# Kernel tuning notes

Measured on AMD Instinct MI355X. Metric: run time of the kernel, lower is better.

The kernel has to match this reference:

```python
import jax, jax.numpy as jnp
import numpy as np

# Block structure (mirrors init_kwargs)
K = 8            # number of blocks
BLK = 1024       # per-block in/out width
TOTAL = K * BLK  # total_dim = 8192
INPUT_IDX = [(i * BLK, (i + 1) * BLK) for i in range(K)]
OUTPUT_IDX = [(((i + 1) % K) * BLK, ((i + 1) % K + 1) * BLK) for i in range(K)]
BATCH = 4096


def setup_inputs() -> dict:
    key = jax.random.key(0)
    k1, k2, k3, k4 = jax.random.split(key, 4)
    x = jax.random.normal(k1, (BATCH, TOTAL), dtype=jnp.float32)
    v = jax.random.normal(k2, (BATCH, TOTAL), dtype=jnp.float32)
    # Per-block Linear params; nn.Linear default init ~ U(-1/sqrt(in), 1/sqrt(in))
    bound = 1.0 / np.sqrt(BLK)
    W = jax.random.uniform(k3, (K, BLK, BLK), dtype=jnp.float32, minval=-bound, maxval=bound)  # [K, out, in]
    b = jax.random.uniform(k4, (K, BLK), dtype=jnp.float32, minval=-bound, maxval=bound)
    return {"x": x, "v": v, "W": W, "b": b}


def reference(x, v, W, b):
    # hidden = act(v)
    hidden = jnp.tanh(v)
    # All input blocks are a uniform partition -> batch the K small GEMMs as one grouped contraction.
    h = hidden.reshape(BATCH, K, BLK)                      # [B, K, in]
    y = jnp.einsum("bki,koi->bko", h, W) + b               # [B, K, out]
    # Scatter-accumulate each block output into its padded position, plus residual x.
    result = x
    for i, (o0, o1) in enumerate(OUTPUT_IDX):
        result = result.at[:, o0:o1].add(y[:, i])
    return result
```

## Files before the change

kernel.cpp:

```cpp
#include <hip/hip_runtime.h>
#include <hip/hip_bf16.h>
#include <stdint.h>

#define BATCH 4096
#define KGRP  8
#define BLK   1024
#define TOTAL 8192

typedef __attribute__((ext_vector_type(8))) short short8;
typedef __attribute__((ext_vector_type(4))) float f32x4;

#define AS1 __attribute__((address_space(1)))
#define AS3 __attribute__((address_space(3)))


__device__ __forceinline__ unsigned short f2bf(float f) {
    union { float f; uint32_t u; } c; c.f = f;
    uint32_t u = c.u;
    u += 0x7fffu + ((u >> 16) & 1u);
    return (unsigned short)(u >> 16);
}

__device__ __forceinline__ float fast_tanh(float x) {
    float e = __expf(2.0f * x);
    return 1.0f - 2.0f / (e + 1.0f);
}


__global__ void k_prep(const float4* __restrict__ v, ushort4* __restrict__ H,
                       const float4* __restrict__ W, ushort4* __restrict__ Wb) {
    const int b = blockIdx.x;
    if (b < 2048) {
        const int n4 = BATCH * TOTAL / 4;
        for (int i = b * 256 + threadIdx.x; i < n4; i += 2048 * 256) {
            float4 f = v[i];
            ushort4 o;
            o.x = f2bf(fast_tanh(f.x)); o.y = f2bf(fast_tanh(f.y));
            o.z = f2bf(fast_tanh(f.z)); o.w = f2bf(fast_tanh(f.w));
            H[i] = o;
        }
    } else {
        const int n4 = KGRP * BLK * BLK / 4;
        for (int i = (b - 2048) * 256 + threadIdx.x; i < n4; i += 512 * 256) {
            float4 f = W[i];
            ushort4 o;
            o.x = f2bf(f.x); o.y = f2bf(f.y); o.z = f2bf(f.z); o.w = f2bf(f.w);
            Wb[i] = o;
        }
    }
}


__device__ __forceinline__ void stage_a(const unsigned short* Asrc0, char* ldsp,
                                        uint32_t bufb, uint32_t sb, int kt, int half) {
#pragma unroll
    for (int h = 0; h < 2; ++h) {
        const int c = half + h * 2;
        __builtin_amdgcn_global_load_lds(
            (const AS1 uint32_t*)(Asrc0 + (size_t)(c * 64) * TOTAL + kt * 64),
            (AS3 uint32_t*)(ldsp + bufb + c * 8192 + sb), 16, 0, 0);
    }
}

__device__ __forceinline__ void stage_b(const unsigned short* Bsrc0, char* ldsp,
                                        uint32_t bufb, uint32_t sb, int kt) {
#pragma unroll
    for (int c = 0; c < 4; ++c) {
        __builtin_amdgcn_global_load_lds(
            (const AS1 uint32_t*)(Bsrc0 + (size_t)(c * 64) * BLK + kt * 64),
            (AS3 uint32_t*)(ldsp + bufb + 32768u + c * 8192 + sb), 16, 0, 0);
    }
}

template<int N> __device__ __forceinline__ void waitvm() {
    if constexpr (N == 0)       asm volatile("s_waitcnt vmcnt(0)" ::: "memory");
    else if constexpr (N == 2)  asm volatile("s_waitcnt vmcnt(2)" ::: "memory");
    else if constexpr (N == 8)  asm volatile("s_waitcnt vmcnt(8)" ::: "memory");
    else if constexpr (N == 12) asm volatile("s_waitcnt vmcnt(12)" ::: "memory");
}

template<int M0>
__device__ __forceinline__ void mfma_phase(const short8 am[2][2], const short8 bfr[4][2],
                                           f32x4 (*acc)[4]) {
    __builtin_amdgcn_s_barrier();
    __builtin_amdgcn_s_setprio(1);
#pragma unroll
    for (int i = 0; i < 2; ++i)
#pragma unroll
        for (int n = 0; n < 4; ++n)
#pragma unroll
            for (int ks = 0; ks < 2; ++ks)
                acc[M0 + i][n] = __builtin_amdgcn_mfma_f32_16x16x32_bf16(am[i][ks], bfr[n][ks], acc[M0 + i][n], 0, 0, 0);
    __builtin_amdgcn_s_setprio(0);
}

template<bool SA13, bool SB, bool SA02, int W1, int W3>
__device__ __forceinline__ void tile_body(int kt, uint32_t bufb, char* ldsp,
                                          uint32_t aRow, uint32_t bRow, const uint32_t* kc,
                                          f32x4 (*acc)[4],
                                          const unsigned short* Asrc0, const unsigned short* Bsrc0,
                                          uint32_t sb) {
    const char* Lb = ldsp + bufb;
    short8 bfr[4][2], am[2][2];

#pragma unroll
    for (int n = 0; n < 4; ++n)
#pragma unroll
        for (int ks = 0; ks < 2; ++ks)
            bfr[n][ks] = *(const short8*)(Lb + bRow + n * 2048 + kc[ks]);
#pragma unroll
    for (int i = 0; i < 2; ++i)
#pragma unroll
        for (int ks = 0; ks < 2; ++ks)
            am[i][ks] = *(const short8*)(Lb + aRow + i * 2048 + kc[ks]);
    if constexpr (SA13) stage_a(Asrc0, ldsp, bufb ^ 65536u, sb, kt + 1, 1);
    mfma_phase<0>(am, bfr, acc);
    __builtin_amdgcn_s_barrier();

#pragma unroll
    for (int i = 0; i < 2; ++i)
#pragma unroll
        for (int ks = 0; ks < 2; ++ks)
            am[i][ks] = *(const short8*)(Lb + aRow + (2 + i) * 2048 + kc[ks]);
    if constexpr (SB) stage_b(Bsrc0, ldsp, bufb, sb, kt + 2);
    mfma_phase<2>(am, bfr, acc);
    waitvm<W1>();
    __builtin_amdgcn_s_barrier();

#pragma unroll
    for (int i = 0; i < 2; ++i)
#pragma unroll
        for (int ks = 0; ks < 2; ++ks)
            am[i][ks] = *(const short8*)(Lb + aRow + (4 + i) * 2048 + kc[ks]);
    if constexpr (SA02) stage_a(Asrc0, ldsp, bufb, sb, kt + 2, 0);
    mfma_phase<4>(am, bfr, acc);
    __builtin_amdgcn_s_barrier();

#pragma unroll
    for (int i = 0; i < 2; ++i)
#pragma unroll
        for (int ks = 0; ks < 2; ++ks)
            am[i][ks] = *(const short8*)(Lb + aRow + (6 + i) * 2048 + kc[ks]);
    mfma_phase<6>(am, bfr, acc);
    if constexpr (W3 >= 0) {
        waitvm<W3>();
        __builtin_amdgcn_s_barrier();
        __builtin_amdgcn_sched_barrier(0);
    }
}

__global__ __launch_bounds__(512, 2)
void k_gemm(const unsigned short* __restrict__ H, const unsigned short* __restrict__ Wb,
            const float* __restrict__ x, const float* __restrict__ bias,
            float* __restrict__ out) {
    __shared__ __attribute__((aligned(1024))) char lds[131072];
    char* ldsp = lds;

    const int bid   = blockIdx.x;
    const int g     = bid & 7;
    const int slot  = bid >> 3;
    const int mtile = slot >> 2;
    const int ntile = slot & 3;

    const int tid  = threadIdx.x;
    const int lane = tid & 63;
    const int w    = tid >> 6;
    const int wr   = w >> 2;
    const int wc   = w & 3;

    uint32_t kc[2];
#pragma unroll
    for (int ks = 0; ks < 2; ++ks)
        kc[ks] = (uint32_t)((ks * 64 + ((lane >> 4) << 4)) ^ ((lane & 7) << 4));
    const uint32_t aRow = (uint32_t)(wr * 128 + (lane & 15)) * 128u;
    const uint32_t bRow = 32768u + (uint32_t)(wc * 64 + (lane & 15)) * 128u;

    const int sRow = tid >> 3;
    const int sCol = (((lane & 7) ^ ((lane >> 3) & 7)) << 3);
    const unsigned short* Asrc0 = H  + ((size_t)(mtile * 256) + sRow) * TOTAL + (size_t)g * BLK + sCol;
    const unsigned short* Bsrc0 = Wb + ((size_t)g * BLK * BLK) + ((size_t)(ntile * 256) + sRow) * BLK + sCol;
    const uint32_t sb = (uint32_t)(w << 10);

    f32x4 acc[8][4];
#pragma unroll
    for (int m = 0; m < 8; ++m)
#pragma unroll
        for (int n = 0; n < 4; ++n) acc[m][n] = (f32x4){0.f, 0.f, 0.f, 0.f};

    stage_b(Bsrc0, ldsp, 0u, sb, 0);
    stage_a(Asrc0, ldsp, 0u, sb, 0, 0);
    stage_a(Asrc0, ldsp, 0u, sb, 0, 1);
    stage_b(Bsrc0, ldsp, 65536u, sb, 1);
    stage_a(Asrc0, ldsp, 65536u, sb, 1, 0);
    waitvm<8>();
    __builtin_amdgcn_s_barrier();
    __builtin_amdgcn_sched_barrier(0);

    uint32_t cur = 0;
#pragma unroll 1
    for (int kt = 0; kt < 14; ++kt) {
        tile_body<true, true, true, 12, 8>(kt, cur << 16, ldsp, aRow, bRow, kc, acc, Asrc0, Bsrc0, sb);
        cur ^= 1u;
    }
    tile_body<true, false, false, 8, 2>(14, cur << 16, ldsp, aRow, bRow, kc, acc, Asrc0, Bsrc0, sb);
    cur ^= 1u;
    tile_body<false, false, false, 0, -1>(15, cur << 16, ldsp, aRow, bRow, kc, acc, Asrc0, Bsrc0, sb);

    const int gout = (g + 1) & 7;
    const int row0 = mtile * 256 + wr * 128 + ((lane >> 4) << 2);
    const int colL = ntile * 256 + wc * 64 + (lane & 15);
    float bv[4];
#pragma unroll
    for (int n = 0; n < 4; ++n) bv[n] = bias[g * BLK + colL + n * 16];
#pragma unroll
    for (int m = 0; m < 8; ++m) {
#pragma unroll
        for (int j = 0; j < 4; ++j) {
            const int row = row0 + m * 16 + j;
            const size_t base = (size_t)row * TOTAL + (size_t)gout * BLK;
#pragma unroll
            for (int n = 0; n < 4; ++n) {
                const size_t idx = base + colL + n * 16;
                out[idx] = x[idx] + bv[n] + acc[m][n][j];
            }
        }
    }
}


__global__ void k_naive(const float* __restrict__ x, const float* __restrict__ v,
                        const float* __restrict__ W, const float* __restrict__ b,
                        float* __restrict__ out) {
    __shared__ float hv[BLK];
    const int bid = blockIdx.x;
    const int quarter = bid & 3;
    const int g = (bid >> 2) & 7;
    const int row = bid >> 5;
    for (int i = threadIdx.x; i < BLK; i += 256)
        hv[i] = tanhf(v[(size_t)row * TOTAL + g * BLK + i]);
    __syncthreads();
    const int o = quarter * 256 + threadIdx.x;
    const float* wrow = W + ((size_t)g * BLK + o) * BLK;
    float s = 0.f;
    for (int i = 0; i < BLK; ++i) s += hv[i] * wrow[i];
    const size_t oi = (size_t)row * TOTAL + (size_t)((g + 1) & 7) * BLK + o;
    out[oi] = x[oi] + b[g * BLK + o] + s;
}


extern "C" void kernel_launch(void* const* d_in, const int* in_sizes, int n_in,
                              void* d_out, int out_size, void* d_ws, size_t ws_size,
                              hipStream_t stream) {
    const float* x = (const float*)d_in[0];
    const float* v = (const float*)d_in[1];
    const float* W = (const float*)d_in[2];
    const float* b = (const float*)d_in[3];
    float* out = (float*)d_out;

    const size_t needH = (size_t)BATCH * TOTAL * sizeof(unsigned short);
    const size_t needW = (size_t)KGRP * BLK * BLK * sizeof(unsigned short);

    if (ws_size >= needH + needW) {
        unsigned short* H  = (unsigned short*)d_ws;
        unsigned short* Wb = (unsigned short*)((char*)d_ws + needH);
        k_prep<<<2560, 256, 0, stream>>>((const float4*)v, (ushort4*)H,
                                         (const float4*)W, (ushort4*)Wb);
        k_gemm<<<512, 512, 0, stream>>>(H, Wb, x, b, out);
    } else {
        k_naive<<<BATCH * KGRP * 4, 256, 0, stream>>>(x, v, W, b, out);
    }
}
```

Baseline: 153.8 us.

## Use 1024-thread blocks with K=32 tiles and LDS-staged coalesced epilogue

The GEMM kernel moves from 512 to 1024 threads per block with a smaller per-wave accumulator tile (4x4 instead of 8x4) and K-step 32 instead of 64, changing the double-buffered LDS staging and swizzle accordingly. The epilogue now transposes accumulators through LDS so each lane writes float4 rows, making the x read and out write coalesced and vectorized. This aims for more waves to hide latency and cheaper output stores, at the cost of twice as many K iterations and barriers, and less data reuse per wave.

```diff
diff --git a/kernel.cpp b/kernel.cpp
--- a/kernel.cpp
+++ b/kernel.cpp
@@ -51,109 +51,64 @@
 }
 
 
-__device__ __forceinline__ void stage_a(const unsigned short* Asrc0, char* ldsp,
-                                        uint32_t bufb, uint32_t sb, int kt, int half) {
-#pragma unroll
-    for (int h = 0; h < 2; ++h) {
-        const int c = half + h * 2;
-        __builtin_amdgcn_global_load_lds(
-            (const AS1 uint32_t*)(Asrc0 + (size_t)(c * 64) * TOTAL + kt * 64),
-            (AS3 uint32_t*)(ldsp + bufb + c * 8192 + sb), 16, 0, 0);
-    }
-}
-
-__device__ __forceinline__ void stage_b(const unsigned short* Bsrc0, char* ldsp,
-                                        uint32_t bufb, uint32_t sb, int kt) {
-#pragma unroll
-    for (int c = 0; c < 4; ++c) {
-        __builtin_amdgcn_global_load_lds(
-            (const AS1 uint32_t*)(Bsrc0 + (size_t)(c * 64) * BLK + kt * 64),
-            (AS3 uint32_t*)(ldsp + bufb + 32768u + c * 8192 + sb), 16, 0, 0);
-    }
+__device__ __forceinline__ void gload16(const unsigned short* src, char* dst) {
+    __builtin_amdgcn_global_load_lds((const AS1 uint32_t*)src, (AS3 uint32_t*)dst, 16, 0, 0);
 }
 
 template<int N> __device__ __forceinline__ void waitvm() {
-    if constexpr (N == 0)       asm volatile("s_waitcnt vmcnt(0)" ::: "memory");
-    else if constexpr (N == 2)  asm volatile("s_waitcnt vmcnt(2)" ::: "memory");
-    else if constexpr (N == 8)  asm volatile("s_waitcnt vmcnt(8)" ::: "memory");
-    else if constexpr (N == 12) asm volatile("s_waitcnt vmcnt(12)" ::: "memory");
-}
-
-template<int M0>
-__device__ __forceinline__ void mfma_phase(const short8 am[2][2], const short8 bfr[4][2],
-                                           f32x4 (*acc)[4]) {
+    if constexpr (N == 0)      asm volatile("s_waitcnt vmcnt(0)" ::: "memory");
+    else if constexpr (N == 1) asm volatile("s_waitcnt vmcnt(1)" ::: "memory");
+    else if constexpr (N == 2) asm volatile("s_waitcnt vmcnt(2)" ::: "memory");
+}
+
+template<bool SA, bool SB, int W>
+__device__ __forceinline__ void tile_body(int kt, char* ldsp,
+                                          uint32_t aRowB, uint32_t bRowB, uint32_t kc,
+                                          f32x4 (*acc)[4],
+                                          const unsigned short* Asrc, const unsigned short* Bsrc,
+                                          uint32_t sdst) {
+    const uint32_t bufb = (uint32_t)(kt & 1) * 32768u;
+    const uint32_t nbuf = bufb ^ 32768u;
+    const char* Lb = ldsp + bufb;
+
+    short8 bfr[4], am[2];
+
+#pragma unroll
+    for (int n = 0; n < 4; ++n)
+        bfr[n] = *(const short8*)(Lb + bRowB + n * 1024 + kc);
+#pragma unroll
+    for (int i = 0; i < 2; ++i)
+        am[i] = *(const short8*)(Lb + aRowB + i * 1024 + kc);
+    if constexpr (SA) gload16(Asrc + (kt + 1) * 32, ldsp + nbuf + sdst);
+#pragma unroll
+    for (int i = 0; i < 2; ++i)
+#pragma unroll
+        for (int n = 0; n < 4; ++n)
+            acc[i][n] = __builtin_amdgcn_mfma_f32_16x16x32_bf16(am[i], bfr[n], acc[i][n], 0, 0, 0);
     __builtin_amdgcn_s_barrier();
-    __builtin_amdgcn_s_setprio(1);
+    __builtin_amdgcn_sched_barrier(0);
+
+#pragma unroll
+    for (int i = 0; i < 2; ++i)
+        am[i] = *(const short8*)(Lb + aRowB + (2 + i) * 1024 + kc);
+    if constexpr (SB) gload16(Bsrc + (kt + 2) * 32, ldsp + bufb + 16384u + sdst);
 #pragma unroll
     for (int i = 0; i < 2; ++i)
 #pragma unroll
         for (int n = 0; n < 4; ++n)
-#pragma unroll
-            for (int ks = 0; ks < 2; ++ks)
-                acc[M0 + i][n] = __builtin_amdgcn_mfma_f32_16x16x32_bf16(am[i][ks], bfr[n][ks], acc[M0 + i][n], 0, 0, 0);
-    __builtin_amdgcn_s_setprio(0);
-}
-
-template<bool SA13, bool SB, bool SA02, int W1, int W3>
-__device__ __forceinline__ void tile_body(int kt, uint32_t bufb, char* ldsp,
-                                          uint32_t aRow, uint32_t bRow, const uint32_t* kc,
-                                          f32x4 (*acc)[4],
-                                          const unsigned short* Asrc0, const unsigned short* Bsrc0,
-                                          uint32_t sb) {
-    const char* Lb = ldsp + bufb;
-    short8 bfr[4][2], am[2][2];
-
-#pragma unroll
-    for (int n = 0; n < 4; ++n)
-#pragma unroll
-        for (int ks = 0; ks < 2; ++ks)
-            bfr[n][ks] = *(const short8*)(Lb + bRow + n * 2048 + kc[ks]);
-#pragma unroll
-    for (int i = 0; i < 2; ++i)
-#pragma unroll
-        for (int ks = 0; ks < 2; ++ks)
-            am[i][ks] = *(const short8*)(Lb + aRow + i * 2048 + kc[ks]);
-    if constexpr (SA13) stage_a(Asrc0, ldsp, bufb ^ 65536u, sb, kt + 1, 1);
-    mfma_phase<0>(am, bfr, acc);
-    __builtin_amdgcn_s_barrier();
-
-#pragma unroll
-    for (int i = 0; i < 2; ++i)
-#pragma unroll
-        for (int ks = 0; ks < 2; ++ks)
-            am[i][ks] = *(const short8*)(Lb + aRow + (2 + i) * 2048 + kc[ks]);
-    if constexpr (SB) stage_b(Bsrc0, ldsp, bufb, sb, kt + 2);
-    mfma_phase<2>(am, bfr, acc);
-    waitvm<W1>();
-    __builtin_amdgcn_s_barrier();
-
-#pragma unroll
-    for (int i = 0; i < 2; ++i)
-#pragma unroll
-        for (int ks = 0; ks < 2; ++ks)
-            am[i][ks] = *(const short8*)(Lb + aRow + (4 + i) * 2048 + kc[ks]);
-    if constexpr (SA02) stage_a(Asrc0, ldsp, bufb, sb, kt + 2, 0);
-    mfma_phase<4>(am, bfr, acc);
-    __builtin_amdgcn_s_barrier();
-
-#pragma unroll
-    for (int i = 0; i < 2; ++i)
-#pragma unroll
-        for (int ks = 0; ks < 2; ++ks)
-            am[i][ks] = *(const short8*)(Lb + aRow + (6 + i) * 2048 + kc[ks]);
-    mfma_phase<6>(am, bfr, acc);
-    if constexpr (W3 >= 0) {
-        waitvm<W3>();
+            acc[2 + i][n] = __builtin_amdgcn_mfma_f32_16x16x32_bf16(am[i], bfr[n], acc[2 + i][n], 0, 0, 0);
+    if constexpr (W >= 0) {
+        waitvm<W>();
         __builtin_amdgcn_s_barrier();
         __builtin_amdgcn_sched_barrier(0);
     }
 }
 
-__global__ __launch_bounds__(512, 2)
+__global__ __launch_bounds__(1024, 4)
 void k_gemm(const unsigned short* __restrict__ H, const unsigned short* __restrict__ Wb,
             const float* __restrict__ x, const float* __restrict__ bias,
             float* __restrict__ out) {
-    __shared__ __attribute__((aligned(1024))) char lds[131072];
+    __shared__ __attribute__((aligned(1024))) char lds[135168];
     char* ldsp = lds;
 
     const int bid   = blockIdx.x;
@@ -168,62 +123,70 @@
     const int wr   = w >> 2;
     const int wc   = w & 3;
 
-    uint32_t kc[2];
-#pragma unroll
-    for (int ks = 0; ks < 2; ++ks)
-        kc[ks] = (uint32_t)((ks * 64 + ((lane >> 4) << 4)) ^ ((lane & 7) << 4));
-    const uint32_t aRow = (uint32_t)(wr * 128 + (lane & 15)) * 128u;
-    const uint32_t bRow = 32768u + (uint32_t)(wc * 64 + (lane & 15)) * 128u;
-
-    const int sRow = tid >> 3;
-    const int sCol = (((lane & 7) ^ ((lane >> 3) & 7)) << 3);
-    const unsigned short* Asrc0 = H  + ((size_t)(mtile * 256) + sRow) * TOTAL + (size_t)g * BLK + sCol;
-    const unsigned short* Bsrc0 = Wb + ((size_t)g * BLK * BLK) + ((size_t)(ntile * 256) + sRow) * BLK + sCol;
-    const uint32_t sb = (uint32_t)(w << 10);
-
-    f32x4 acc[8][4];
-#pragma unroll
-    for (int m = 0; m < 8; ++m)
+    const uint32_t kc    = ((uint32_t)((lane >> 4) ^ ((lane >> 1) & 3))) << 4;
+    const uint32_t aRowB = (uint32_t)(wr * 64 + (lane & 15)) * 64u;
+    const uint32_t bRowB = 16384u + (uint32_t)(wc * 64 + (lane & 15)) * 64u;
+
+    const int sCol = ((lane & 3) ^ ((lane >> 3) & 3)) << 3;
+    const unsigned short* Asrc = H + (size_t)(mtile * 256 + w * 16 + (lane >> 2)) * TOTAL
+                                   + (size_t)g * BLK + sCol;
+    const unsigned short* Bsrc = Wb + (size_t)g * BLK * BLK
+                                    + (size_t)(ntile * 256 + w * 16 + (lane >> 2)) * BLK + sCol;
+    const uint32_t sdst = (uint32_t)(w << 10);
+
+    f32x4 acc[4][4];
+#pragma unroll
+    for (int m = 0; m < 4; ++m)
 #pragma unroll
         for (int n = 0; n < 4; ++n) acc[m][n] = (f32x4){0.f, 0.f, 0.f, 0.f};
 
-    stage_b(Bsrc0, ldsp, 0u, sb, 0);
-    stage_a(Asrc0, ldsp, 0u, sb, 0, 0);
-    stage_a(Asrc0, ldsp, 0u, sb, 0, 1);
-    stage_b(Bsrc0, ldsp, 65536u, sb, 1);
-    stage_a(Asrc0, ldsp, 65536u, sb, 1, 0);
-    waitvm<8>();
+    gload16(Asrc + 0 * 32, ldsp + 0u + sdst);
+    gload16(Bsrc + 0 * 32, ldsp + 16384u + sdst);
+    gload16(Asrc + 1 * 32, ldsp + 32768u + sdst);
+    gload16(Bsrc + 1 * 32, ldsp + 32768u + 16384u + sdst);
+    waitvm<2>();
     __builtin_amdgcn_s_barrier();
     __builtin_amdgcn_sched_barrier(0);
 
-    uint32_t cur = 0;
+    tile_body<false, true, 1>(0, ldsp, aRowB, bRowB, kc, acc, Asrc, Bsrc, sdst);
 #pragma unroll 1
-    for (int kt = 0; kt < 14; ++kt) {
-        tile_body<true, true, true, 12, 8>(kt, cur << 16, ldsp, aRow, bRow, kc, acc, Asrc0, Bsrc0, sb);
-        cur ^= 1u;
-    }
-    tile_body<true, false, false, 8, 2>(14, cur << 16, ldsp, aRow, bRow, kc, acc, Asrc0, Bsrc0, sb);
-    cur ^= 1u;
-    tile_body<false, false, false, 0, -1>(15, cur << 16, ldsp, aRow, bRow, kc, acc, Asrc0, Bsrc0, sb);
+    for (int kt = 1; kt < 30; ++kt)
+        tile_body<true, true, 1>(kt, ldsp, aRowB, bRowB, kc, acc, Asrc, Bsrc, sdst);
+    tile_body<true, false, 0>(30, ldsp, aRowB, bRowB, kc, acc, Asrc, Bsrc, sdst);
+    tile_body<false, false, -1>(31, ldsp, aRowB, bRowB, kc, acc, Asrc, Bsrc, sdst);
 
     const int gout = (g + 1) & 7;
-    const int row0 = mtile * 256 + wr * 128 + ((lane >> 4) << 2);
-    const int colL = ntile * 256 + wc * 64 + (lane & 15);
-    float bv[4];
-#pragma unroll
-    for (int n = 0; n < 4; ++n) bv[n] = bias[g * BLK + colL + n * 16];
-#pragma unroll
-    for (int m = 0; m < 8; ++m) {
-#pragma unroll
-        for (int j = 0; j < 4; ++j) {
-            const int row = row0 + m * 16 + j;
-            const size_t base = (size_t)row * TOTAL + (size_t)gout * BLK;
-#pragma unroll
-            for (int n = 0; n < 4; ++n) {
-                const size_t idx = base + colL + n * 16;
-                out[idx] = x[idx] + bv[n] + acc[m][n][j];
-            }
+    const int q    = lane >> 4;
+    const int cl   = lane & 15;
+    const int row0 = mtile * 256 + wr * 64;
+    const int col0 = ntile * 256 + wc * 64;
+    char* eb = ldsp + 65536u + (uint32_t)w * 4352u;
+    const float4 bias4 = *(const float4*)&bias[g * BLK + col0 + cl * 4];
+
+#pragma unroll
+    for (int m = 0; m < 4; ++m) {
+#pragma unroll
+        for (int n = 0; n < 4; ++n)
+#pragma unroll
+            for (int j = 0; j < 4; ++j)
+                *(float*)(eb + (q * 4 + j) * 272 + (n * 16 + cl) * 4) = acc[m][n][j];
+        asm volatile("s_waitcnt lgkmcnt(0)" ::: "memory");
+        __builtin_amdgcn_sched_barrier(0);
+#pragma unroll
+        for (int i = 0; i < 4; ++i) {
+            f32x4 vv = *(const f32x4*)(eb + (q + 4 * i) * 272 + cl * 16);
+            const int r = row0 + m * 16 + q + 4 * i;
+            const size_t idx = (size_t)r * TOTAL + (size_t)gout * BLK + col0 + cl * 4;
+            const float4 xv = *(const float4*)&x[idx];
+            float4 o;
+            o.x = xv.x + bias4.x + vv[0];
+            o.y = xv.y + bias4.y + vv[1];
+            o.z = xv.z + bias4.z + vv[2];
+            o.w = xv.w + bias4.w + vv[3];
+            *(float4*)&out[idx] = o;
         }
+        asm volatile("s_waitcnt lgkmcnt(0)" ::: "memory");
+        __builtin_amdgcn_sched_barrier(0);
     }
 }
 
@@ -265,7 +228,7 @@
         unsigned short* Wb = (unsigned short*)((char*)d_ws + needH);
         k_prep<<<2560, 256, 0, stream>>>((const float4*)v, (ushort4*)H,
                                          (const float4*)W, (ushort4*)Wb);
-        k_gemm<<<512, 512, 0, stream>>>(H, Wb, x, b, out);
+        k_gemm<<<512, 1024, 0, stream>>>(H, Wb, x, b, out);
     } else {
         k_naive<<<BATCH * KGRP * 4, 256, 0, stream>>>(x, v, W, b, out);
     }
```

After: 158.8 us. 3.2% more time.
